# Optimization experiments

Hardware: AMD Instinct MI355X
Metric: run time of the kernel (lower is better)

The kernel has to match this reference:

```python
import jax, jax.numpy as jnp
import numpy as np

EMBED_DIM = 1024
NUM_HEADS = 16
HEAD_DIM = EMBED_DIM // NUM_HEADS


def setup_inputs() -> dict:
    key = jax.random.key(0)
    ks = jax.random.split(key, 6)
    s = 1.0 / np.sqrt(EMBED_DIM)
    x = jax.random.normal(ks[0], (2, 2048, EMBED_DIM), dtype=jnp.float32)
    Wk = jax.random.uniform(ks[1], (EMBED_DIM, EMBED_DIM), jnp.float32, -s, s)
    Wq = jax.random.uniform(ks[2], (EMBED_DIM, EMBED_DIM), jnp.float32, -s, s)
    Wv = jax.random.uniform(ks[3], (EMBED_DIM, EMBED_DIM), jnp.float32, -s, s)
    Wo = jax.random.uniform(ks[4], (EMBED_DIM, EMBED_DIM), jnp.float32, -s, s)
    bo = jax.random.uniform(ks[5], (EMBED_DIM,), jnp.float32, -s, s)
    return {"x": x, "Wq": Wq, "Wk": Wk, "Wv": Wv, "Wo": Wo, "bo": bo}


def reference(x, Wq, Wk, Wv, Wo, bo):
    b, s, e = x.shape
    h, d = NUM_HEADS, HEAD_DIM
    scale = d ** (-0.5)
    # nn.Linear: y = x @ W.T ; here W stored as [out, in] -> use W.T
    q = (x @ Wq.T).reshape(b, s, h, d).transpose(0, 2, 1, 3)  # b h s d
    k = (x @ Wk.T).reshape(b, s, h, d).transpose(0, 2, 1, 3)
    v = (x @ Wv.T).reshape(b, s, h, d).transpose(0, 2, 1, 3)
    logits = jnp.einsum('bhqd,bhkd->bhqk', q, k) * scale
    attn = jax.nn.softmax(logits, axis=-1)
    out = jnp.einsum('bhqk,bhkd->bhqd', attn, v)
    out = out.transpose(0, 2, 1, 3).reshape(b, s, e)
    return out @ Wo.T + bo
```

## Files before the change

kernel.cpp:

```cpp
#include <hip/hip_runtime.h>
#include <hip/hip_bf16.h>

using short8 = __attribute__((ext_vector_type(8))) short;
using f32x4  = __attribute__((ext_vector_type(4))) float;
using uint4v = __attribute__((ext_vector_type(4))) unsigned;

#if __has_builtin(__builtin_amdgcn_exp2f)
#define EXP2(x) __builtin_amdgcn_exp2f(x)
#else
#define EXP2(x) exp2f(x)
#endif

__device__ __forceinline__ short f2bf(float f) {
    union { float f; unsigned u; } v; v.f = f;
    unsigned r = v.u + 0x7fffu + ((v.u >> 16) & 1u);
    return (short)(r >> 16);
}
__device__ __forceinline__ unsigned pack_trunc(float a, float b) {
    union { float f; unsigned u; } ua, ub; ua.f = a; ub.f = b;
#if __has_builtin(__builtin_amdgcn_perm)
    return __builtin_amdgcn_perm(ub.u, ua.u, 0x07060302u);
#else
    return (ub.u & 0xFFFF0000u) | (ua.u >> 16);
#endif
}
__device__ __forceinline__ void async_copy16(const short* g, short* s) {
    __builtin_amdgcn_global_load_lds(
        (const __attribute__((address_space(1))) void*)g,
        (__attribute__((address_space(3))) void*)s, 16, 0, 0);
}

__global__ __launch_bounds__(256) void cvt_f32_bf16(
    const float* __restrict__ s0, const float* __restrict__ s1,
    const float* __restrict__ s2, const float* __restrict__ s3,
    const float* __restrict__ s4,
    short* __restrict__ d0, short* __restrict__ d1, short* __restrict__ d2,
    short* __restrict__ d3, short* __restrict__ d4,
    int n0, int n1, int n2, int n3, int n4) {
    const float* s; short* d; int n;
    switch (blockIdx.y) {
        case 0: s = s0; d = d0; n = n0; break;
        case 1: s = s1; d = d1; n = n1; break;
        case 2: s = s2; d = d2; n = n2; break;
        case 3: s = s3; d = d3; n = n3; break;
        default: s = s4; d = d4; n = n4; break;
    }
    const int idx = (blockIdx.x * 256 + threadIdx.x) * 4;
    if (idx < n) {
        float4 v = *(const float4*)(s + idx);
        short4 o;
        o.x = f2bf(v.x); o.y = f2bf(v.y); o.z = f2bf(v.z); o.w = f2bf(v.w);
        *(short4*)(d + idx) = o;
    }
}

template <int MODE>
__device__ __forceinline__ void gemm_body(const short* __restrict__ A,
                                          const short* __restrict__ B,
                                          short* __restrict__ C,
                                          float scale) {
    constexpr int Kd = 1024, Nd = 1024, Sd = 2048;
    __shared__ __align__(16) short As[128 * 32];
    __shared__ __align__(16) short Bs[128 * 32];

    const int tid  = threadIdx.x;
    const int w    = tid >> 6, lane = tid & 63;
    const int quad = lane >> 4, l16 = lane & 15;
    const int wm   = (w >> 1) * 64, wn = (w & 1) * 64;
    const int bm   = blockIdx.y * 128, bn = blockIdx.x * 128;

    f32x4 acc[4][4];
#pragma unroll
    for (int i = 0; i < 4; ++i)
#pragma unroll
        for (int j = 0; j < 4; ++j) acc[i][j] = (f32x4){0.f, 0.f, 0.f, 0.f};

    for (int k0 = 0; k0 < Kd; k0 += 32) {
        __syncthreads();
#pragma unroll
        for (int c = 0; c < 2; ++c) {
            int li  = c * 256 + tid;
            int row = li >> 2;
            int col = (li & 3) * 8;
            async_copy16(A + (size_t)(bm + row) * Kd + k0 + col, &As[li * 8]);
            async_copy16(B + (size_t)(bn + row) * Kd + k0 + col, &Bs[li * 8]);
        }
        __syncthreads();

        short8 af[4], bfv[4];
#pragma unroll
        for (int mi = 0; mi < 4; ++mi)
            af[mi] = *(const short8*)(&As[(wm + mi * 16 + l16) * 32 + quad * 8]);
#pragma unroll
        for (int ni = 0; ni < 4; ++ni)
            bfv[ni] = *(const short8*)(&Bs[(wn + ni * 16 + l16) * 32 + quad * 8]);
#pragma unroll
        for (int mi = 0; mi < 4; ++mi)
#pragma unroll
            for (int ni = 0; ni < 4; ++ni) {
                if constexpr (MODE == 2)
                    acc[mi][ni] = __builtin_amdgcn_mfma_f32_16x16x32_bf16(
                        bfv[ni], af[mi], acc[mi][ni], 0, 0, 0);
                else
                    acc[mi][ni] = __builtin_amdgcn_mfma_f32_16x16x32_bf16(
                        af[mi], bfv[ni], acc[mi][ni], 0, 0, 0);
            }
    }

    if constexpr (MODE == 2) {
#pragma unroll
        for (int mi = 0; mi < 4; ++mi) {
            const int m_g = bm + wm + mi * 16 + l16;
            const int b_  = m_g >> 11, s_ = m_g & 2047;
#pragma unroll
            for (int ni = 0; ni < 4; ++ni)
#pragma unroll
                for (int r = 0; r < 4; ++r) {
                    const int n_g = bn + wn + ni * 16 + quad * 4 + r;
                    C[(size_t)b_ * Nd * Sd + (size_t)n_g * Sd + s_] =
                        f2bf(acc[mi][ni][r]);
                }
        }
    } else {
#pragma unroll
        for (int ni = 0; ni < 4; ++ni) {
            const int colg = bn + wn + ni * 16 + l16;
#pragma unroll
            for (int mi = 0; mi < 4; ++mi)
#pragma unroll
                for (int r = 0; r < 4; ++r) {
                    const int rowg = bm + wm + mi * 16 + quad * 4 + r;
                    C[(size_t)rowg * Nd + colg] = f2bf(acc[mi][ni][r] * scale);
                }
        }
    }
}

#define CSC 0.18033688f

__global__ __launch_bounds__(256, 2) void proj_gemm(
    const short* __restrict__ X,
    const short* __restrict__ Wq, const short* __restrict__ Wk,
    const short* __restrict__ Wv,
    short* __restrict__ Qo, short* __restrict__ Ko, short* __restrict__ VTo) {
    if (blockIdx.z == 0)
        gemm_body<0>(X, Wq, Qo, CSC);
    else if (blockIdx.z == 1)
        gemm_body<0>(X, Wk, Ko, 1.0f);
    else
        gemm_body<2>(X, Wv, VTo, 1.0f);
}

__global__ __launch_bounds__(256, 2) void out_gemm(
    const short* __restrict__ A, const short* __restrict__ B,
    const float* __restrict__ bias, float* __restrict__ C) {
    constexpr int Kd = 1024, Nd = 1024;
    __shared__ __align__(16) short As[64 * 32];
    __shared__ __align__(16) short Bs[128 * 32];

    const int tid  = threadIdx.x;
    const int w    = tid >> 6, lane = tid & 63;
    const int quad = lane >> 4, l16 = lane & 15;
    const int wm   = (w >> 1) * 32, wn = (w & 1) * 64;
    const int bm   = blockIdx.y * 64, bn = blockIdx.x * 128;

    f32x4 acc[2][4];
#pragma unroll
    for (int i = 0; i < 2; ++i)
#pragma unroll
        for (int j = 0; j < 4; ++j) acc[i][j] = (f32x4){0.f, 0.f, 0.f, 0.f};

    for (int k0 = 0; k0 < Kd; k0 += 32) {
        __syncthreads();
        {
            int row = tid >> 2, col = (tid & 3) * 8;
            async_copy16(A + (size_t)(bm + row) * Kd + k0 + col, &As[tid * 8]);
        }
#pragma unroll
        for (int c = 0; c < 2; ++c) {
            int li  = c * 256 + tid;
            int row = li >> 2;
            int col = (li & 3) * 8;
            async_copy16(B + (size_t)(bn + row) * Kd + k0 + col, &Bs[li * 8]);
        }
        __syncthreads();

        short8 af[2], bfv[4];
#pragma unroll
        for (int mi = 0; mi < 2; ++mi)
            af[mi] = *(const short8*)(&As[(wm + mi * 16 + l16) * 32 + quad * 8]);
#pragma unroll
        for (int ni = 0; ni < 4; ++ni)
            bfv[ni] = *(const short8*)(&Bs[(wn + ni * 16 + l16) * 32 + quad * 8]);
#pragma unroll
        for (int mi = 0; mi < 2; ++mi)
#pragma unroll
            for (int ni = 0; ni < 4; ++ni)
                acc[mi][ni] = __builtin_amdgcn_mfma_f32_16x16x32_bf16(
                    af[mi], bfv[ni], acc[mi][ni], 0, 0, 0);
    }

#pragma unroll
    for (int ni = 0; ni < 4; ++ni) {
        const int colg = bn + wn + ni * 16 + l16;
        const float bv = bias[colg];
#pragma unroll
        for (int mi = 0; mi < 2; ++mi)
#pragma unroll
            for (int r = 0; r < 4; ++r) {
                const int rowg = bm + wm + mi * 16 + quad * 4 + r;
                C[(size_t)rowg * Nd + colg] = acc[mi][ni][r] + bv;
            }
    }
}

__global__ __launch_bounds__(256, 2) void attn_kernel(
    const short* __restrict__ Q, const short* __restrict__ K,
    const short* __restrict__ VT, short* __restrict__ O) {
    constexpr int S = 2048, E = 1024, NT = S / 64;
    __shared__ __align__(16) short Ks[2][64 * 64];
    __shared__ __align__(16) short Vs[2][64 * 64];

    const int tid  = threadIdx.x;
    const int w    = tid >> 6, lane = tid & 63;
    const int quad = lane >> 4, l16 = lane & 15;
    const int bh   = blockIdx.y, b = bh >> 4, h = bh & 15;
    const int qt   = blockIdx.x;

    const int    q0   = qt * 128 + w * 32;
    const size_t base = (size_t)b * S * E;
    const size_t vtb  = (size_t)b * E * S;
    const int    hc   = h * 64;
    const int    xr   = l16 & 7;

    short8 aq[2][2];
#pragma unroll
    for (int qg = 0; qg < 2; ++qg) {
        const short* qp = Q + base + (size_t)(q0 + qg * 16 + l16) * E + hc + quad * 8;
        aq[qg][0] = *(const short8*)(qp);
        aq[qg][1] = *(const short8*)(qp + 32);
    }

    f32x4 oT[2][4], o_sum[2];
#pragma unroll
    for (int qg = 0; qg < 2; ++qg) {
        o_sum[qg] = (f32x4){0.f, 0.f, 0.f, 0.f};
#pragma unroll
        for (int i = 0; i < 4; ++i) oT[qg][i] = (f32x4){0.f, 0.f, 0.f, 0.f};
    }

    int          kdst[2], vdst0[2], vdst1[2];
    const short* kga[2];
    const short* vga[2];
#pragma unroll
    for (int c = 0; c < 2; ++c) {
        int li = c * 256 + tid, row = li >> 3, cc = li & 7;
        kdst[c] = row * 64 + ((cc ^ (row & 7)) * 8);
        int c0   = 4 * (cc >> 2) + 2 * (cc & 1);
        int boff = 4 * ((cc >> 1) & 1);
        vdst0[c] = row * 64 + ((c0 ^ (row & 7)) * 8) + boff;
        vdst1[c] = row * 64 + (((c0 + 1) ^ (row & 7)) * 8) + boff;
        kga[c]   = K + base + (size_t)row * E + hc + cc * 8;
        vga[c]   = VT + vtb + (size_t)(hc + row) * S + cc * 8;
    }

    short8 kr[2], vr[2];
#pragma unroll
    for (int c = 0; c < 2; ++c) {
        kr[c] = *(const short8*)(kga[c]);
        vr[c] = *(const short8*)(vga[c]);
    }
#pragma unroll
    for (int c = 0; c < 2; ++c) {
        *(short8*)(&Ks[0][kdst[c]]) = kr[c];
        short4 lo, hi;
        lo.x = vr[c][0]; lo.y = vr[c][1]; lo.z = vr[c][2]; lo.w = vr[c][3];
        hi.x = vr[c][4]; hi.y = vr[c][5]; hi.z = vr[c][6]; hi.w = vr[c][7];
        *(short4*)(&Vs[0][vdst0[c]]) = lo;
        *(short4*)(&Vs[0][vdst1[c]]) = hi;
    }
#pragma unroll
    for (int c = 0; c < 2; ++c) {
        kr[c] = *(const short8*)(kga[c] + (size_t)64 * E);
        vr[c] = *(const short8*)(vga[c] + 64);
    }
    __syncthreads();

    const short8 ones = (short8){0x3F80, 0x3F80, 0x3F80, 0x3F80,
                                 0x3F80, 0x3F80, 0x3F80, 0x3F80};
    const float  LB   = 0.00281502f;

    for (int kt = 0; kt < NT; ++kt) {
        const int    cur = kt & 1;
        const short* Kc  = Ks[cur];
        const short* Vc  = Vs[cur];

        if (kt + 1 < NT) {
            short* Kn = Ks[cur ^ 1];
            short* Vn = Vs[cur ^ 1];
#pragma unroll
            for (int c = 0; c < 2; ++c) {
                *(short8*)(&Kn[kdst[c]]) = kr[c];
                short4 lo, hi;
                lo.x = vr[c][0]; lo.y = vr[c][1]; lo.z = vr[c][2]; lo.w = vr[c][3];
                hi.x = vr[c][4]; hi.y = vr[c][5]; hi.z = vr[c][6]; hi.w = vr[c][7];
                *(short4*)(&Vn[vdst0[c]]) = lo;
                *(short4*)(&Vn[vdst1[c]]) = hi;
            }
            if (kt + 2 < NT) {
#pragma unroll
                for (int c = 0; c < 2; ++c) {
                    kr[c] = *(const short8*)(kga[c] + (size_t)(kt + 2) * 64 * E);
                    vr[c] = *(const short8*)(vga[c] + (kt + 2) * 64);
                }
            }
        }

        uint4v pkv[2][2];
#pragma unroll
        for (int kn = 0; kn < 4; ++kn) {
            const short* kb  = &Kc[(kn * 16 + l16) * 64];
            short8       bk0 = *(const short8*)(kb + ((quad ^ xr) * 8));
            short8       bk1 = *(const short8*)(kb + (((quad + 4) ^ xr) * 8));
#pragma unroll
            for (int qg = 0; qg < 2; ++qg) {
                f32x4 a = (f32x4){LB, LB, LB, LB};
                a = __builtin_amdgcn_mfma_f32_16x16x32_bf16(bk0, aq[qg][0], a, 0, 0, 0);
                a = __builtin_amdgcn_mfma_f32_16x16x32_bf16(bk1, aq[qg][1], a, 0, 0, 0);
                pkv[qg][kn >> 1][(kn & 1) * 2]     = pack_trunc(EXP2(a[0]), EXP2(a[1]));
                pkv[qg][kn >> 1][(kn & 1) * 2 + 1] = pack_trunc(EXP2(a[2]), EXP2(a[3]));
            }
        }

#pragma unroll
        for (int ks = 0; ks < 2; ++ks) {
            short8 pf[2];
#pragma unroll
            for (int qg = 0; qg < 2; ++qg) {
                union { uint4v u; short8 s; } cv;
                cv.u   = pkv[qg][ks];
                pf[qg] = cv.s;
                o_sum[qg] = __builtin_amdgcn_mfma_f32_16x16x32_bf16(
                    ones, pf[qg], o_sum[qg], 0, 0, 0);
            }
#pragma unroll
            for (int ni = 0; ni < 4; ++ni) {
                const int rv = ni * 16 + l16;
                short8 vb =
                    *(const short8*)(&Vc[rv * 64 + (((ks * 4 + quad) ^ xr) * 8)]);
#pragma unroll
                for (int qg = 0; qg < 2; ++qg)
                    oT[qg][ni] = __builtin_amdgcn_mfma_f32_16x16x32_bf16(
                        vb, pf[qg], oT[qg][ni], 0, 0, 0);
            }
        }
        __syncthreads();
    }

#pragma unroll
    for (int qg = 0; qg < 2; ++qg) {
        const float inv = 1.0f / o_sum[qg][0];
        const int   qg_ = q0 + qg * 16 + l16;
#pragma unroll
        for (int ni = 0; ni < 4; ++ni) {
            short4 ov;
            ov.x = f2bf(oT[qg][ni][0] * inv);
            ov.y = f2bf(oT[qg][ni][1] * inv);
            ov.z = f2bf(oT[qg][ni][2] * inv);
            ov.w = f2bf(oT[qg][ni][3] * inv);
            *(short4*)(&O[base + (size_t)qg_ * E + hc + ni * 16 + quad * 4]) = ov;
        }
    }
}

extern "C" void kernel_launch(void* const* d_in, const int* in_sizes, int n_in,
                              void* d_out, int out_size, void* d_ws, size_t ws_size,
                              hipStream_t stream) {
    const float* x  = (const float*)d_in[0];
    const float* Wq = (const float*)d_in[1];
    const float* Wk = (const float*)d_in[2];
    const float* Wv = (const float*)d_in[3];
    const float* Wo = (const float*)d_in[4];
    const float* bo = (const float*)d_in[5];
    float* out = (float*)d_out;

    constexpr int XN = 2 * 2048 * 1024;
    constexpr int WN = 1024 * 1024;

    short* Xb  = (short*)d_ws;
    short* Wqb = Xb + XN;
    short* Wkb = Wqb + WN;
    short* Wvb = Wkb + WN;
    short* Wob = Wvb + WN;
    short* Qb  = Wob + WN;
    short* Kb  = Qb + XN;
    short* VTb = Kb + XN;

    cvt_f32_bf16<<<dim3(4096, 5), 256, 0, stream>>>(
        x, Wq, Wk, Wv, Wo, Xb, Wqb, Wkb, Wvb, Wob, XN, WN, WN, WN, WN);
    proj_gemm<<<dim3(8, 32, 3), 256, 0, stream>>>(Xb, Wqb, Wkb, Wvb, Qb, Kb, VTb);
    attn_kernel<<<dim3(16, 32), 256, 0, stream>>>(Qb, Kb, VTb, Xb );
    out_gemm<<<dim3(8, 64), 256, 0, stream>>>(Xb, Wob, bo, out);
}
```

Baseline: 177.6 us.

## Double GEMM K-tile to 64 with XOR-swizzled shared memory layout

Both projection and output GEMMs now stage a 64-wide K slice per iteration instead of 32, which halves the number of barrier pairs and loop iterations. The global-to-LDS copy permutes the 16-byte chunks by an XOR with the row index, and the fragment reads apply the same XOR so that LDS bank conflicts are avoided on the wider rows. proj_gemm's launch bounds are raised to 3 blocks per CU, which may constrain registers. LDS use per block doubles, and that could limit occupancy.

```diff
diff --git a/kernel.cpp b/kernel.cpp
--- a/kernel.cpp
+++ b/kernel.cpp
@@ -60,12 +60,13 @@
                                           short* __restrict__ C,
                                           float scale) {
     constexpr int Kd = 1024, Nd = 1024, Sd = 2048;
-    __shared__ __align__(16) short As[128 * 32];
-    __shared__ __align__(16) short Bs[128 * 32];
+    __shared__ __align__(16) short As[128 * 64];
+    __shared__ __align__(16) short Bs[128 * 64];
 
     const int tid  = threadIdx.x;
     const int w    = tid >> 6, lane = tid & 63;
     const int quad = lane >> 4, l16 = lane & 15;
+    const int xr   = l16 & 7;
     const int wm   = (w >> 1) * 64, wn = (w & 1) * 64;
     const int bm   = blockIdx.y * 128, bn = blockIdx.x * 128;
 
@@ -75,36 +76,45 @@
 #pragma unroll
         for (int j = 0; j < 4; ++j) acc[i][j] = (f32x4){0.f, 0.f, 0.f, 0.f};
 
-    for (int k0 = 0; k0 < Kd; k0 += 32) {
+    for (int k0 = 0; k0 < Kd; k0 += 64) {
         __syncthreads();
 #pragma unroll
-        for (int c = 0; c < 2; ++c) {
-            int li  = c * 256 + tid;
-            int row = li >> 2;
-            int col = (li & 3) * 8;
-            async_copy16(A + (size_t)(bm + row) * Kd + k0 + col, &As[li * 8]);
-            async_copy16(B + (size_t)(bn + row) * Kd + k0 + col, &Bs[li * 8]);
+        for (int c = 0; c < 4; ++c) {
+            int li   = c * 256 + tid;
+            int row  = li >> 3;
+            int gcol = ((li & 7) ^ (row & 7)) * 8;
+            async_copy16(A + (size_t)(bm + row) * Kd + k0 + gcol, &As[li * 8]);
+            async_copy16(B + (size_t)(bn + row) * Kd + k0 + gcol, &Bs[li * 8]);
         }
         __syncthreads();
 
-        short8 af[4], bfv[4];
-#pragma unroll
-        for (int mi = 0; mi < 4; ++mi)
-            af[mi] = *(const short8*)(&As[(wm + mi * 16 + l16) * 32 + quad * 8]);
-#pragma unroll
-        for (int ni = 0; ni < 4; ++ni)
-            bfv[ni] = *(const short8*)(&Bs[(wn + ni * 16 + l16) * 32 + quad * 8]);
-#pragma unroll
-        for (int mi = 0; mi < 4; ++mi)
+#pragma unroll
+        for (int kk = 0; kk < 2; ++kk) {
+            short8 af[4], bfv[4];
+#pragma unroll
+            for (int mi = 0; mi < 4; ++mi) {
+                const int r = wm + mi * 16 + l16;
+                af[mi] = *(const short8*)(
+                    &As[r * 64 + (((kk * 4 + quad) ^ xr) * 8)]);
+            }
 #pragma unroll
             for (int ni = 0; ni < 4; ++ni) {
-                if constexpr (MODE == 2)
-                    acc[mi][ni] = __builtin_amdgcn_mfma_f32_16x16x32_bf16(
-                        bfv[ni], af[mi], acc[mi][ni], 0, 0, 0);
-                else
-                    acc[mi][ni] = __builtin_amdgcn_mfma_f32_16x16x32_bf16(
-                        af[mi], bfv[ni], acc[mi][ni], 0, 0, 0);
-            }
+                const int r = wn + ni * 16 + l16;
+                bfv[ni] = *(const short8*)(
+                    &Bs[r * 64 + (((kk * 4 + quad) ^ xr) * 8)]);
+            }
+#pragma unroll
+            for (int mi = 0; mi < 4; ++mi)
+#pragma unroll
+                for (int ni = 0; ni < 4; ++ni) {
+                    if constexpr (MODE == 2)
+                        acc[mi][ni] = __builtin_amdgcn_mfma_f32_16x16x32_bf16(
+                            bfv[ni], af[mi], acc[mi][ni], 0, 0, 0);
+                    else
+                        acc[mi][ni] = __builtin_amdgcn_mfma_f32_16x16x32_bf16(
+                            af[mi], bfv[ni], acc[mi][ni], 0, 0, 0);
+                }
+        }
     }
 
     if constexpr (MODE == 2) {
@@ -138,7 +148,7 @@
 
 #define CSC 0.18033688f
 
-__global__ __launch_bounds__(256, 2) void proj_gemm(
+__global__ __launch_bounds__(256, 3) void proj_gemm(
     const short* __restrict__ X,
     const short* __restrict__ Wq, const short* __restrict__ Wk,
     const short* __restrict__ Wv,
@@ -155,12 +165,13 @@
     const short* __restrict__ A, const short* __restrict__ B,
     const float* __restrict__ bias, float* __restrict__ C) {
     constexpr int Kd = 1024, Nd = 1024;
-    __shared__ __align__(16) short As[64 * 32];
-    __shared__ __align__(16) short Bs[128 * 32];
+    __shared__ __align__(16) short As[64 * 64];
+    __shared__ __align__(16) short Bs[128 * 64];
 
     const int tid  = threadIdx.x;
     const int w    = tid >> 6, lane = tid & 63;
     const int quad = lane >> 4, l16 = lane & 15;
+    const int xr   = l16 & 7;
     const int wm   = (w >> 1) * 32, wn = (w & 1) * 64;
     const int bm   = blockIdx.y * 64, bn = blockIdx.x * 128;
 
@@ -170,34 +181,46 @@
 #pragma unroll
         for (int j = 0; j < 4; ++j) acc[i][j] = (f32x4){0.f, 0.f, 0.f, 0.f};
 
-    for (int k0 = 0; k0 < Kd; k0 += 32) {
+    for (int k0 = 0; k0 < Kd; k0 += 64) {
         __syncthreads();
-        {
-            int row = tid >> 2, col = (tid & 3) * 8;
-            async_copy16(A + (size_t)(bm + row) * Kd + k0 + col, &As[tid * 8]);
-        }
 #pragma unroll
         for (int c = 0; c < 2; ++c) {
-            int li  = c * 256 + tid;
-            int row = li >> 2;
-            int col = (li & 3) * 8;
-            async_copy16(B + (size_t)(bn + row) * Kd + k0 + col, &Bs[li * 8]);
+            int li   = c * 256 + tid;
+            int row  = li >> 3;
+            int gcol = ((li & 7) ^ (row & 7)) * 8;
+            async_copy16(A + (size_t)(bm + row) * Kd + k0 + gcol, &As[li * 8]);
+        }
+#pragma unroll
+        for (int c = 0; c < 4; ++c) {
+            int li   = c * 256 + tid;
+            int row  = li >> 3;
+            int gcol = ((li & 7) ^ (row & 7)) * 8;
+            async_copy16(B + (size_t)(bn + row) * Kd + k0 + gcol, &Bs[li * 8]);
         }
         __syncthreads();
 
-        short8 af[2], bfv[4];
-#pragma unroll
-        for (int mi = 0; mi < 2; ++mi)
-            af[mi] = *(const short8*)(&As[(wm + mi * 16 + l16) * 32 + quad * 8]);
-#pragma unroll
-        for (int ni = 0; ni < 4; ++ni)
-            bfv[ni] = *(const short8*)(&Bs[(wn + ni * 16 + l16) * 32 + quad * 8]);
-#pragma unroll
-        for (int mi = 0; mi < 2; ++mi)
-#pragma unroll
-            for (int ni = 0; ni < 4; ++ni)
-                acc[mi][ni] = __builtin_amdgcn_mfma_f32_16x16x32_bf16(
-                    af[mi], bfv[ni], acc[mi][ni], 0, 0, 0);
+#pragma unroll
+        for (int kk = 0; kk < 2; ++kk) {
+            short8 af[2], bfv[4];
+#pragma unroll
+            for (int mi = 0; mi < 2; ++mi) {
+                const int r = wm + mi * 16 + l16;
+                af[mi] = *(const short8*)(
+                    &As[r * 64 + (((kk * 4 + quad) ^ xr) * 8)]);
+            }
+#pragma unroll
+            for (int ni = 0; ni < 4; ++ni) {
+                const int r = wn + ni * 16 + l16;
+                bfv[ni] = *(const short8*)(
+                    &Bs[r * 64 + (((kk * 4 + quad) ^ xr) * 8)]);
+            }
+#pragma unroll
+            for (int mi = 0; mi < 2; ++mi)
+#pragma unroll
+                for (int ni = 0; ni < 4; ++ni)
+                    acc[mi][ni] = __builtin_amdgcn_mfma_f32_16x16x32_bf16(
+                        af[mi], bfv[ni], acc[mi][ni], 0, 0, 0);
+        }
     }
 
 #pragma unroll
```

Result: slower. 184.0 us (+3.6%).
